# Kernel tuning notes

Hardware: AMD Instinct MI355X
Metric: run time of the kernel (lower is better)

Reference implementation:

```python
import jax, jax.numpy as jnp
import numpy as np

DIM = 1024
HEADS = 16
HEAD_DIM = DIM // HEADS


def setup_inputs() -> dict:
    key = jax.random.key(0)
    ks = jax.random.split(key, 9)
    s = 1.0 / np.sqrt(DIM)
    return {
        "x": jax.random.normal(ks[0], (2, 2048, 1, DIM), dtype=jnp.float32),
        "Wq": jax.random.normal(ks[1], (DIM, DIM), dtype=jnp.float32) * s,
        "bq": jnp.zeros((DIM,), dtype=jnp.float32),
        "Wk": jax.random.normal(ks[2], (DIM, DIM), dtype=jnp.float32) * s,
        "bk": jnp.zeros((DIM,), dtype=jnp.float32),
        "Wv": jax.random.normal(ks[3], (DIM, DIM), dtype=jnp.float32) * s,
        "bv": jnp.zeros((DIM,), dtype=jnp.float32),
        "Wo": jax.random.normal(ks[4], (DIM, DIM), dtype=jnp.float32) * s,
        "bo": jnp.zeros((DIM,), dtype=jnp.float32),
    }


def reference(x, Wq, bq, Wk, bk, Wv, bv, Wo, bo):
    b, t, _, d = x.shape
    h, hd = HEADS, HEAD_DIM
    # torch Linear: y = x @ W.T + b
    q = (x @ Wq.T + bq).reshape(b, t, h, hd)
    k = (x @ Wk.T + bk).reshape(b, t, h, hd)
    v = (x @ Wv.T + bv).reshape(b, t, h, hd)
    # Source applies self.scaling (hd**-0.5) in torch AND divides by
    # sqrt(k_features) inside the jax chunk routine -> net scale 1/hd.
    q = q * (1.0 / hd)
    # key_chunk_size >= T -> one chunk; online softmax == exact stable softmax
    scores = jnp.einsum('bqhd,bkhd->bhqk', q, k)  # [B,H,T,T]
    w = jax.nn.softmax(scores, axis=-1)
    o = jnp.einsum('bhqk,bkhd->bqhd', w, v).reshape(b, t, d)
    return o @ Wo.T + bo
```

## Files before the change

### kernel.cpp

```cpp
#include <hip/hip_runtime.h>
#include <math.h>

typedef _Float16 f16;
typedef _Float16 f16x2 __attribute__((ext_vector_type(2)));
typedef _Float16 f16x4 __attribute__((ext_vector_type(4)));
typedef _Float16 f16x8 __attribute__((ext_vector_type(8)));
typedef float    f32x4 __attribute__((ext_vector_type(4)));

constexpr int DIM   = 1024;
constexpr int HEADS = 16;
constexpr int HD    = 64;
constexpr int BATCH = 2;
constexpr int SEQ   = 2048;
constexpr int MTOT  = BATCH * SEQ;
constexpr int NT2   = SEQ / 128;

#define QSCALE (1.4426950408889634f / 64.0f)

#define MFMA16(a, b, c) __builtin_amdgcn_mfma_f32_16x16x32_f16((a), (b), (c), 0, 0, 0)
#define SPLIT2(x, hh, ll) { const float _t = (x); hh = (f16)_t; ll = (f16)(_t - (float)(hh)); }

__device__ __forceinline__ void glds16(const void* g, void* l) {
    __builtin_amdgcn_global_load_lds(
        (const __attribute__((address_space(1))) void*)g,
        (__attribute__((address_space(3))) void*)l, 16, 0, 0);
}

__device__ __forceinline__ float exp2_hw(float x) {
    float r;
    asm("v_exp_f32 %0, %1" : "=v"(r) : "v"(x));
    return r;
}

__device__ __forceinline__ f16x2 pk_f16(float a, float b) {
    return __builtin_bit_cast(f16x2, __builtin_amdgcn_cvt_pkrtz(a, b));
}

__global__ __launch_bounds__(256) void presplit_kernel(
    const float* __restrict__ x,  const float* __restrict__ Wq,
    const float* __restrict__ Wk, const float* __restrict__ Wv,
    const float* __restrict__ Wo,
    f16* __restrict__ Xh,  f16* __restrict__ WqH, f16* __restrict__ WkH,
    f16* __restrict__ WvH, f16* __restrict__ WoH, f16* __restrict__ WoL)
{
    const int bid = blockIdx.x;
    const float* src; f16* dh; f16* dl = nullptr; int row;
    if (bid < 4096)      { src = x;  dh = Xh;  row = bid; }
    else if (bid < 5120) { src = Wq; dh = WqH; row = bid - 4096; }
    else if (bid < 6144) { src = Wk; dh = WkH; row = bid - 5120; }
    else if (bid < 7168) { src = Wv; dh = WvH; row = bid - 6144; }
    else                 { src = Wo; dh = WoH; dl = WoL; row = bid - 7168; }

    const int k = threadIdx.x * 4;
    const float4 v = *reinterpret_cast<const float4*>(&src[(size_t)row * DIM + k]);
    const int s = (row >> 1) & 3;
    const size_t o = (size_t)row * DIM + (k & ~31) + ((k & 31) ^ (s << 3));
    if (dl) {
        f16x4 h4, l4;
        SPLIT2(v.x, h4[0], l4[0]); SPLIT2(v.y, h4[1], l4[1]);
        SPLIT2(v.z, h4[2], l4[2]); SPLIT2(v.w, h4[3], l4[3]);
        *reinterpret_cast<f16x4*>(&dh[o]) = h4;
        *reinterpret_cast<f16x4*>(&dl[o]) = l4;
    } else {
        f16x4 h4;
        h4[0] = (f16)v.x; h4[1] = (f16)v.y; h4[2] = (f16)v.z; h4[3] = (f16)v.w;
        *reinterpret_cast<f16x4*>(&dh[o]) = h4;
    }
}

template <int MODE, int TERMS>
__device__ __forceinline__ void gemm_plane_body(
    const f16* __restrict__ AhG, const f16* __restrict__ BhG,
    const f16* __restrict__ BlG, const float* __restrict__ bias,
    float* __restrict__ C, f16* __restrict__ F, float scale,
    f16* __restrict__ smem)
{
    f16* Ah = smem;
    f16* Bh = smem + 4096;
    f16* Bl = smem + 8192;

    const int tid = threadIdx.x;
    const int l   = tid & 63;
    const int w   = tid >> 6;
    const int wm  = (w >> 1) * 64;
    const int wn  = (w & 1) * 64;
    const int m0  = blockIdx.y * 128;
    const int n0  = blockIdx.x * 128;
    const int fr  = l & 15;
    const int fk  = (l >> 4) * 8;
    const int rg  = (l >> 4) * 4;
    const int fko = fk ^ (((fr >> 1) & 3) << 3);

    f32x4 acc[4][4] = {};

    for (int k0 = 0; k0 < DIM; k0 += 32) {
        __syncthreads();
        constexpr int NCH = (TERMS == 1) ? 4 : 6;
        #pragma unroll
        for (int j = 0; j < NCH; ++j) {
            const int c = w * NCH + j;
            const int p = c >> 3;
            const f16* P = (p == 0) ? AhG : (p == 1) ? BhG : BlG;
            const int r0 = (p == 0) ? m0 : n0;
            const int row = r0 + (c & 7) * 16 + (l >> 2);
            glds16(P + (size_t)row * DIM + k0 + (l & 3) * 8, smem + c * 512);
        }
        asm volatile("s_waitcnt vmcnt(0)" ::: "memory");
        __syncthreads();

        f16x8 ah[4], bh[4], bl[4];
        #pragma unroll
        for (int m = 0; m < 4; ++m)
            ah[m] = *reinterpret_cast<const f16x8*>(&Ah[(wm + m * 16 + fr) * 32 + fko]);
        #pragma unroll
        for (int n = 0; n < 4; ++n) {
            const int r = (wn + n * 16 + fr) * 32 + fko;
            bh[n] = *reinterpret_cast<const f16x8*>(&Bh[r]);
            if (TERMS == 2) bl[n] = *reinterpret_cast<const f16x8*>(&Bl[r]);
        }
        #pragma unroll
        for (int n = 0; n < 4; ++n) {
            #pragma unroll
            for (int m = 0; m < 4; ++m) {
                if (MODE == 1) {
                    acc[m][n] = MFMA16(bh[n], ah[m], acc[m][n]);
                } else {
                    acc[m][n] = MFMA16(ah[m], bh[n], acc[m][n]);
                    if (TERMS == 2)
                        acc[m][n] = MFMA16(ah[m], bl[n], acc[m][n]);
                }
            }
        }
    }

    if (MODE == 0 || MODE == 3) {
        #pragma unroll
        for (int n = 0; n < 4; ++n) {
            const int col  = n0 + wn + n * 16 + fr;
            const float bb = bias[col];
            #pragma unroll
            for (int m = 0; m < 4; ++m) {
                #pragma unroll
                for (int r = 0; r < 4; ++r) {
                    const int row = m0 + wm + m * 16 + rg + r;
                    const float v = (acc[m][n][r] + bb) * scale;
                    if (MODE == 0) C[(size_t)row * DIM + col] = v;
                    else           F[(size_t)row * DIM + col] = (f16)v;
                }
            }
        }
    } else if (MODE == 1) {
        constexpr int RS = 72;
        const int batch = m0 >> 11;
        const int kvg0  = m0 & 2047;
        for (int s = 0; s < 2; ++s) {
            __syncthreads();
            if ((w & 1) == s) {
                #pragma unroll
                for (int n = 0; n < 4; ++n) {
                    #pragma unroll
                    for (int m = 0; m < 4; ++m) {
                        const int kvrow = wm + m * 16 + fr;
                        const int dd    = n * 16 + rg;
                        f16x4 h4;
                        #pragma unroll
                        for (int r = 0; r < 4; ++r)
                            h4[r] = (f16)(acc[m][n][r] + bias[n0 + wn + dd + r]);
                        const int o = kvrow * RS + (dd ^ ((kvrow & 7) << 3));
                        *reinterpret_cast<f16x4*>(&smem[o]) = h4;
                    }
                }
            }
            __syncthreads();
            const size_t bh_ = (size_t)batch * HEADS + (n0 >> 6) + s;
            const int row = tid >> 1, c0 = (tid & 1) * 32;
            #pragma unroll
            for (int j = 0; j < 4; ++j) {
                const int so = row * RS + c0 + j * 8;
                const size_t go = bh_ * 131072 + (size_t)(kvg0 + row) * 64 + c0 + j * 8;
                *reinterpret_cast<f16x8*>(&F[go]) =
                    *reinterpret_cast<const f16x8*>(&smem[so]);
            }
        }
    } else {
        constexpr int RS = 136;
        const int batch = m0 >> 11;
        const int kvg0  = m0 & 2047;
        for (int s = 0; s < 2; ++s) {
            __syncthreads();
            if ((w & 1) == s) {
                #pragma unroll
                for (int n = 0; n < 4; ++n) {
                    const int d    = n * 16 + fr;
                    const float bb = bias[n0 + wn + d];
                    #pragma unroll
                    for (int m = 0; m < 4; ++m) {
                        const int kvl = wm + m * 16 + rg;
                        f16x4 h4;
                        h4[0] = (f16)(acc[m][n][0] + bb);
                        h4[1] = (f16)(acc[m][n][1] + bb);
                        h4[2] = (f16)(acc[m][n][2] + bb);
                        h4[3] = (f16)(acc[m][n][3] + bb);
                        const int o = d * RS + (kvl ^ ((d & 7) << 3));
                        *reinterpret_cast<f16x4*>(&smem[o]) = h4;
                    }
                }
            }
            __syncthreads();
            const size_t bh_ = (size_t)batch * HEADS + (n0 >> 6) + s;
            const int row = tid >> 2, c0 = (tid & 3) * 32;
            #pragma unroll
            for (int j = 0; j < 4; ++j) {
                const int so = row * RS + c0 + j * 8;
                const size_t go = bh_ * 131072 + (size_t)row * 2048 + kvg0 + c0 + j * 8;
                *reinterpret_cast<f16x8*>(&F[go]) =
                    *reinterpret_cast<const f16x8*>(&smem[so]);
            }
        }
    }
}

__global__ __launch_bounds__(256) void qkv_kernel(
    const f16* __restrict__ XhG,
    const f16* __restrict__ WqH, const float* __restrict__ bq,
    const f16* __restrict__ WkH, const float* __restrict__ bk,
    const f16* __restrict__ WvH, const float* __restrict__ bv,
    f16* __restrict__ QhG, f16* __restrict__ KhG, f16* __restrict__ VhG)
{
    __shared__ __align__(16) f16 smem[9216];
    if (blockIdx.z == 0)
        gemm_plane_body<3, 1>(XhG, WqH, nullptr, bq, nullptr, QhG, QSCALE, smem);
    else if (blockIdx.z == 1)
        gemm_plane_body<1, 1>(XhG, WkH, nullptr, bk, nullptr, KhG, 1.0f, smem);
    else
        gemm_plane_body<2, 1>(XhG, WvH, nullptr, bv, nullptr, VhG, 1.0f, smem);
}

__global__ __launch_bounds__(256) void oproj_kernel(
    const f16* __restrict__ OhG,
    const f16* __restrict__ WoH, const f16* __restrict__ WoL,
    const float* __restrict__ bo, float* __restrict__ out)
{
    __shared__ __align__(16) f16 smem[12288];
    gemm_plane_body<0, 2>(OhG, WoH, WoL, bo, out, nullptr, 1.0f, smem);
}

__global__ __launch_bounds__(256, 2) void attn_kernel(
    const f16* __restrict__ QhG, const f16* __restrict__ KhG,
    const f16* __restrict__ VhG, f16* __restrict__ OhG)
{
    __shared__ __align__(16) f16 lds[2][2][8192];
    __shared__ __align__(16) f16 PL[4][2][1024];

    const int tid = threadIdx.x;
    const int l   = tid & 63;
    const int w   = tid >> 6;
    const int fr  = l & 15;
    const int g   = l >> 4;
    const int fk  = g * 8;
    const int rg  = g * 4;
    const int swz = (fr & 7) << 3;

    const int lin  = blockIdx.x + 16 * (blockIdx.y + 16 * blockIdx.z);
    const int sid  = (lin & 7) * 64 + (lin >> 3);
    const int qblk = sid & 15;
    const int head = (sid >> 4) & 15;
    const int batch = sid >> 8;

    const int q0 = qblk * 128;
    const size_t rowbase = (size_t)batch * SEQ;
    const int hcol = head * HD;
    const size_t bhbase = ((size_t)batch * HEADS + head) * (size_t)(SEQ * HD);

    size_t kA[4], vA[4];
    #pragma unroll
    for (int c = 0; c < 4; ++c) {
        const int h0 = (w * 4 + c) * 512 + l * 8;
        kA[c] = bhbase + (size_t)h0;
        vA[c] = bhbase + (size_t)(h0 >> 7) * 2048 + (h0 & 127);
    }

#define STAGE(B, T) do {                                                    \
        const size_t _ko = (size_t)(T) * 8192;                              \
        const size_t _vo = (size_t)(T) * 128;                               \
        _Pragma("unroll")                                                   \
        for (int c = 0; c < 4; ++c) {                                       \
            const int lo_ = (w * 4 + c) * 512;                              \
            glds16(KhG + kA[c] + _ko, &lds[B][0][lo_]);                     \
            glds16(VhG + vA[c] + _vo, &lds[B][1][lo_]);                     \
        }                                                                   \
    } while (0)

    STAGE(0, 0);

    f16x8 qh[2][2];
    #pragma unroll
    for (int qb = 0; qb < 2; ++qb) {
        const f16* qp = &QhG[(rowbase + q0 + w * 32 + qb * 16 + fr) * DIM + hcol];
        qh[qb][0] = *reinterpret_cast<const f16x8*>(&qp[fk]);
        qh[qb][1] = *reinterpret_cast<const f16x8*>(&qp[32 + fk]);
    }

    f16x8 onesv;
    #pragma unroll
    for (int i = 0; i < 8; ++i) onesv[i] = (f16)1.0f;

    f32x4 ls[2] = {};
    f32x4 oa[4][2] = {};

    int cur = 0;
    for (int t = 0; t < NT2; ++t) {
        asm volatile("s_waitcnt vmcnt(0) lgkmcnt(0)\ns_barrier" ::: "memory");
        if (t + 1 < NT2) STAGE(cur ^ 1, t + 1);

        #pragma unroll
        for (int hh = 0; hh < 2; ++hh) {
            const f16* Kh = &lds[cur][0][hh * 4096];
            const f16* Vh = &lds[cur][1][hh * 64];

            f32x4 sa[4][2] = {};
            __builtin_amdgcn_s_setprio(1);
            #pragma unroll
            for (int kvb = 0; kvb < 4; ++kvb) {
                #pragma unroll
                for (int ks = 0; ks < 2; ++ks) {
                    const int o = ((kvb * 16 + fr) * 64 + ks * 32 + fk) ^ swz;
                    const f16x8 kh = *reinterpret_cast<const f16x8*>(&Kh[o]);
                    sa[kvb][0] = MFMA16(kh, qh[0][ks], sa[kvb][0]);
                    sa[kvb][1] = MFMA16(kh, qh[1][ks], sa[kvb][1]);
                }
            }
            __builtin_amdgcn_s_setprio(0);

            f16x8 pf[2][2];
            #pragma unroll
            for (int qb = 0; qb < 2; ++qb) {
                f16* Wh = &PL[w][qb][0];
                #pragma unroll
                for (int kvb = 0; kvb < 4; ++kvb) {
                    const f16x2 p01 = pk_f16(exp2_hw(sa[kvb][qb][0]),
                                             exp2_hw(sa[kvb][qb][1]));
                    const f16x2 p23 = pk_f16(exp2_hw(sa[kvb][qb][2]),
                                             exp2_hw(sa[kvb][qb][3]));
                    f16x4 h4;
                    h4[0] = p01[0]; h4[1] = p01[1]; h4[2] = p23[0]; h4[3] = p23[1];
                    const int po = (fr * 64 + kvb * 16 + rg) ^ swz;
                    *reinterpret_cast<f16x4*>(&Wh[po]) = h4;
                }
                #pragma unroll
                for (int ks = 0; ks < 2; ++ks) {
                    const int ro = (fr * 64 + ks * 32 + fk) ^ swz;
                    pf[qb][ks] = *reinterpret_cast<const f16x8*>(&Wh[ro]);
                }
            }

            __builtin_amdgcn_s_setprio(1);
            #pragma unroll
            for (int qb = 0; qb < 2; ++qb)
                #pragma unroll
                for (int ks = 0; ks < 2; ++ks)
                    ls[qb] = MFMA16(onesv, pf[qb][ks], ls[qb]);
            #pragma unroll
            for (int db = 0; db < 4; ++db) {
                #pragma unroll
                for (int ks = 0; ks < 2; ++ks) {
                    const int vo = (db * 16 + fr) * 128 + ((ks * 32 + fk) ^ swz);
                    const f16x8 vh = *reinterpret_cast<const f16x8*>(&Vh[vo]);
                    oa[db][0] = MFMA16(vh, pf[0][ks], oa[db][0]);
                    oa[db][1] = MFMA16(vh, pf[1][ks], oa[db][1]);
                }
            }
            __builtin_amdgcn_s_setprio(0);
        }
        cur ^= 1;
    }
#undef STAGE

    #pragma unroll
    for (int qb = 0; qb < 2; ++qb) {
        const float inv = 1.0f / ls[qb][0];
        const size_t row = rowbase + q0 + w * 32 + qb * 16 + fr;
        const int s = ((int)row >> 1) & 3;
        #pragma unroll
        for (int db = 0; db < 4; ++db) {
            f16x4 h4;
            #pragma unroll
            for (int j = 0; j < 4; ++j) h4[j] = (f16)(oa[db][qb][j] * inv);
            const int kg = hcol + db * 16 + rg;
            const size_t o = row * DIM + (kg & ~31) + ((kg & 31) ^ (s << 3));
            *reinterpret_cast<f16x4*>(&OhG[o]) = h4;
        }
    }
}

extern "C" void kernel_launch(void* const* d_in, const int* in_sizes, int n_in,
                              void* d_out, int out_size, void* d_ws, size_t ws_size,
                              hipStream_t stream)
{
    const float* x  = (const float*)d_in[0];
    const float* Wq = (const float*)d_in[1];
    const float* bq = (const float*)d_in[2];
    const float* Wk = (const float*)d_in[3];
    const float* bk = (const float*)d_in[4];
    const float* Wv = (const float*)d_in[5];
    const float* bv = (const float*)d_in[6];
    const float* Wo = (const float*)d_in[7];
    const float* bo = (const float*)d_in[8];
    float* out = (float*)d_out;

    const size_t PS = (size_t)MTOT * DIM;
    f16* QhG = (f16*)d_ws;
    f16* KhG = QhG + PS;
    f16* VhG = KhG + PS;
    f16* XhG = VhG + PS;
    f16* WqH = XhG + PS;
    f16* WkH = WqH + (size_t)DIM * DIM;
    f16* WvH = WkH + (size_t)DIM * DIM;
    f16* WoH = WvH + (size_t)DIM * DIM;
    f16* WoL = WoH + (size_t)DIM * DIM;
    f16* OhG = XhG;

    presplit_kernel<<<8192, 256, 0, stream>>>(x, Wq, Wk, Wv, Wo,
                                              XhG, WqH, WkH, WvH, WoH, WoL);

    dim3 gqkv(DIM / 128, MTOT / 128, 3);
    qkv_kernel<<<gqkv, 256, 0, stream>>>(XhG, WqH, bq, WkH, bk, WvH, bv,
                                         QhG, KhG, VhG);

    dim3 gattn(SEQ / 128, HEADS, BATCH);
    attn_kernel<<<gattn, 256, 0, stream>>>(QhG, KhG, VhG, OhG);

    dim3 gout(DIM / 128, MTOT / 128);
    oproj_kernel<<<gout, 256, 0, stream>>>(OhG, WoH, WoL, bo, out);
}
```

Baseline: 125.9 us.

## Double-buffer LDS tiles in projection GEMM main loop

Restructures the shared GEMM body used by the QKV and output projections so the next K-slice is loaded asynchronously into a second LDS buffer while MFMAs run on the current one. One barrier per iteration replaces the previous two, and global-load latency can overlap with compute. In exchange it doubles LDS per block for both kernels, which may reduce occupancy.

```diff
diff --git a/kernel.cpp b/kernel.cpp
--- a/kernel.cpp
+++ b/kernel.cpp
@@ -75,9 +75,8 @@
     float* __restrict__ C, f16* __restrict__ F, float scale,
     f16* __restrict__ smem)
 {
-    f16* Ah = smem;
-    f16* Bh = smem + 4096;
-    f16* Bl = smem + 8192;
+    constexpr int NCH  = (TERMS == 1) ? 4 : 6;
+    constexpr int BUFH = NCH * 4 * 512;
 
     const int tid = threadIdx.x;
     const int l   = tid & 63;
@@ -93,20 +92,29 @@
 
     f32x4 acc[4][4] = {};
 
+#define GSTAGE(B, K0) do {                                                  \
+        _Pragma("unroll")                                                   \
+        for (int j = 0; j < NCH; ++j) {                                     \
+            const int c = w * NCH + j;                                      \
+            const int p = c >> 3;                     \
+            const f16* P = (p == 0) ? AhG : (p == 1) ? BhG : BlG;           \
+            const int r0 = (p == 0) ? m0 : n0;                              \
+            const int row = r0 + (c & 7) * 16 + (l >> 2);                   \
+            glds16(P + (size_t)row * DIM + (K0) + (l & 3) * 8,              \
+                   smem + (B) * BUFH + c * 512);                            \
+        }                                                                   \
+    } while (0)
+
+    GSTAGE(0, 0);
+    asm volatile("s_waitcnt vmcnt(0)\ns_barrier" ::: "memory");
+    int cur = 0;
+
     for (int k0 = 0; k0 < DIM; k0 += 32) {
-        __syncthreads();
-        constexpr int NCH = (TERMS == 1) ? 4 : 6;
-        #pragma unroll
-        for (int j = 0; j < NCH; ++j) {
-            const int c = w * NCH + j;
-            const int p = c >> 3;
-            const f16* P = (p == 0) ? AhG : (p == 1) ? BhG : BlG;
-            const int r0 = (p == 0) ? m0 : n0;
-            const int row = r0 + (c & 7) * 16 + (l >> 2);
-            glds16(P + (size_t)row * DIM + k0 + (l & 3) * 8, smem + c * 512);
-        }
-        asm volatile("s_waitcnt vmcnt(0)" ::: "memory");
-        __syncthreads();
+        if (k0 + 32 < DIM) GSTAGE(cur ^ 1, k0 + 32);
+
+        const f16* Ah = smem + cur * BUFH;
+        const f16* Bh = Ah + 4096;
+        const f16* Bl = Bh + 4096;
 
         f16x8 ah[4], bh[4], bl[4];
         #pragma unroll
@@ -131,7 +139,10 @@
                 }
             }
         }
-    }
+        asm volatile("s_waitcnt vmcnt(0) lgkmcnt(0)\ns_barrier" ::: "memory");
+        cur ^= 1;
+    }
+#undef GSTAGE
 
     if (MODE == 0 || MODE == 3) {
         #pragma unroll
@@ -227,7 +238,7 @@
     const f16* __restrict__ WvH, const float* __restrict__ bv,
     f16* __restrict__ QhG, f16* __restrict__ KhG, f16* __restrict__ VhG)
 {
-    __shared__ __align__(16) f16 smem[9216];
+    __shared__ __align__(16) f16 smem[18432];
     if (blockIdx.z == 0)
         gemm_plane_body<3, 1>(XhG, WqH, nullptr, bq, nullptr, QhG, QSCALE, smem);
     else if (blockIdx.z == 1)
@@ -241,7 +252,7 @@
     const f16* __restrict__ WoH, const f16* __restrict__ WoL,
     const float* __restrict__ bo, float* __restrict__ out)
 {
-    __shared__ __align__(16) f16 smem[12288];
+    __shared__ __align__(16) f16 smem[24576];
     gemm_plane_body<0, 2>(OhG, WoH, WoL, bo, out, nullptr, 1.0f, smem);
 }
 
```

Result: slower. 132.2 us (+5.0%).

## Drop split-fp16 Wo low term and deepen GEMM K-tile to 64

Applied to the files above, without the earlier changes.

The output projection no longer keeps a high/low fp16 split of Wo. It now uses only the fp16 high part, which halves the MFMA count and removes the WoL buffer and its writes in the presplit kernel. The shared GEMM body also moves from a K-step of 32 to 64, loading twice as much per iteration into larger LDS tiles to halve the number of barrier/wait rounds. The cost is lower output-projection precision and more LDS use per block, with a possible rise in bank conflicts from the wider 64-element row stride.

```diff
diff --git a/kernel.cpp b/kernel.cpp
--- a/kernel.cpp
+++ b/kernel.cpp
@@ -18,7 +18,6 @@
 #define QSCALE (1.4426950408889634f / 64.0f)
 
 #define MFMA16(a, b, c) __builtin_amdgcn_mfma_f32_16x16x32_f16((a), (b), (c), 0, 0, 0)
-#define SPLIT2(x, hh, ll) { const float _t = (x); hh = (f16)_t; ll = (f16)(_t - (float)(hh)); }
 
 __device__ __forceinline__ void glds16(const void* g, void* l) {
     __builtin_amdgcn_global_load_lds(
@@ -41,43 +40,33 @@
     const float* __restrict__ Wk, const float* __restrict__ Wv,
     const float* __restrict__ Wo,
     f16* __restrict__ Xh,  f16* __restrict__ WqH, f16* __restrict__ WkH,
-    f16* __restrict__ WvH, f16* __restrict__ WoH, f16* __restrict__ WoL)
+    f16* __restrict__ WvH, f16* __restrict__ WoH)
 {
     const int bid = blockIdx.x;
-    const float* src; f16* dh; f16* dl = nullptr; int row;
+    const float* src; f16* dh; int row;
     if (bid < 4096)      { src = x;  dh = Xh;  row = bid; }
     else if (bid < 5120) { src = Wq; dh = WqH; row = bid - 4096; }
     else if (bid < 6144) { src = Wk; dh = WkH; row = bid - 5120; }
     else if (bid < 7168) { src = Wv; dh = WvH; row = bid - 6144; }
-    else                 { src = Wo; dh = WoH; dl = WoL; row = bid - 7168; }
+    else                 { src = Wo; dh = WoH; row = bid - 7168; }
 
     const int k = threadIdx.x * 4;
     const float4 v = *reinterpret_cast<const float4*>(&src[(size_t)row * DIM + k]);
     const int s = (row >> 1) & 3;
     const size_t o = (size_t)row * DIM + (k & ~31) + ((k & 31) ^ (s << 3));
-    if (dl) {
-        f16x4 h4, l4;
-        SPLIT2(v.x, h4[0], l4[0]); SPLIT2(v.y, h4[1], l4[1]);
-        SPLIT2(v.z, h4[2], l4[2]); SPLIT2(v.w, h4[3], l4[3]);
-        *reinterpret_cast<f16x4*>(&dh[o]) = h4;
-        *reinterpret_cast<f16x4*>(&dl[o]) = l4;
-    } else {
-        f16x4 h4;
-        h4[0] = (f16)v.x; h4[1] = (f16)v.y; h4[2] = (f16)v.z; h4[3] = (f16)v.w;
-        *reinterpret_cast<f16x4*>(&dh[o]) = h4;
-    }
-}
-
-template <int MODE, int TERMS>
+    f16x4 h4;
+    h4[0] = (f16)v.x; h4[1] = (f16)v.y; h4[2] = (f16)v.z; h4[3] = (f16)v.w;
+    *reinterpret_cast<f16x4*>(&dh[o]) = h4;
+}
+
+template <int MODE>
 __device__ __forceinline__ void gemm_plane_body(
     const f16* __restrict__ AhG, const f16* __restrict__ BhG,
-    const f16* __restrict__ BlG, const float* __restrict__ bias,
-    float* __restrict__ C, f16* __restrict__ F, float scale,
-    f16* __restrict__ smem)
+    const float* __restrict__ bias, float* __restrict__ C,
+    f16* __restrict__ F, float scale, f16* __restrict__ smem)
 {
     f16* Ah = smem;
-    f16* Bh = smem + 4096;
-    f16* Bl = smem + 8192;
+    f16* Bh = smem + 8192;
 
     const int tid = threadIdx.x;
     const int l   = tid & 63;
@@ -93,44 +82,44 @@
 
     f32x4 acc[4][4] = {};
 
-    for (int k0 = 0; k0 < DIM; k0 += 32) {
+    for (int k0 = 0; k0 < DIM; k0 += 64) {
         __syncthreads();
-        constexpr int NCH = (TERMS == 1) ? 4 : 6;
-        #pragma unroll
-        for (int j = 0; j < NCH; ++j) {
-            const int c = w * NCH + j;
-            const int p = c >> 3;
-            const f16* P = (p == 0) ? AhG : (p == 1) ? BhG : BlG;
+        #pragma unroll
+        for (int j = 0; j < 8; ++j) {
+            const int c  = w * 8 + j;
+            const int p  = c >> 4;
+            const int cc = c & 15;
+            const f16* P = (p == 0) ? AhG : BhG;
             const int r0 = (p == 0) ? m0 : n0;
-            const int row = r0 + (c & 7) * 16 + (l >> 2);
-            glds16(P + (size_t)row * DIM + k0 + (l & 3) * 8, smem + c * 512);
+            const int row = r0 + cc * 8 + (l >> 3);
+            glds16(P + (size_t)row * DIM + k0 + (l & 7) * 8, smem + c * 512);
         }
         asm volatile("s_waitcnt vmcnt(0)" ::: "memory");
         __syncthreads();
 
-        f16x8 ah[4], bh[4], bl[4];
-        #pragma unroll
-        for (int m = 0; m < 4; ++m)
-            ah[m] = *reinterpret_cast<const f16x8*>(&Ah[(wm + m * 16 + fr) * 32 + fko]);
-        #pragma unroll
-        for (int n = 0; n < 4; ++n) {
-            const int r = (wn + n * 16 + fr) * 32 + fko;
-            bh[n] = *reinterpret_cast<const f16x8*>(&Bh[r]);
-            if (TERMS == 2) bl[n] = *reinterpret_cast<const f16x8*>(&Bl[r]);
-        }
-        #pragma unroll
-        for (int n = 0; n < 4; ++n) {
-            #pragma unroll
-            for (int m = 0; m < 4; ++m) {
-                if (MODE == 1) {
-                    acc[m][n] = MFMA16(bh[n], ah[m], acc[m][n]);
-                } else {
-                    acc[m][n] = MFMA16(ah[m], bh[n], acc[m][n]);
-                    if (TERMS == 2)
-                        acc[m][n] = MFMA16(ah[m], bl[n], acc[m][n]);
-                }
-            }
-        }
+        f16x8 ah[2][4], bh[2][4];
+        #pragma unroll
+        for (int ks = 0; ks < 2; ++ks) {
+            #pragma unroll
+            for (int m = 0; m < 4; ++m)
+                ah[ks][m] = *reinterpret_cast<const f16x8*>(
+                    &Ah[(wm + m * 16 + fr) * 64 + ks * 32 + fko]);
+            #pragma unroll
+            for (int n = 0; n < 4; ++n)
+                bh[ks][n] = *reinterpret_cast<const f16x8*>(
+                    &Bh[(wn + n * 16 + fr) * 64 + ks * 32 + fko]);
+        }
+        #pragma unroll
+        for (int ks = 0; ks < 2; ++ks)
+            #pragma unroll
+            for (int n = 0; n < 4; ++n)
+                #pragma unroll
+                for (int m = 0; m < 4; ++m) {
+                    if (MODE == 1)
+                        acc[m][n] = MFMA16(bh[ks][n], ah[ks][m], acc[m][n]);
+                    else
+                        acc[m][n] = MFMA16(ah[ks][m], bh[ks][n], acc[m][n]);
+                }
     }
 
     if (MODE == 0 || MODE == 3) {
@@ -227,22 +216,21 @@
     const f16* __restrict__ WvH, const float* __restrict__ bv,
     f16* __restrict__ QhG, f16* __restrict__ KhG, f16* __restrict__ VhG)
 {
-    __shared__ __align__(16) f16 smem[9216];
+    __shared__ __align__(16) f16 smem[18432];
     if (blockIdx.z == 0)
-        gemm_plane_body<3, 1>(XhG, WqH, nullptr, bq, nullptr, QhG, QSCALE, smem);
+        gemm_plane_body<3>(XhG, WqH, bq, nullptr, QhG, QSCALE, smem);
     else if (blockIdx.z == 1)
-        gemm_plane_body<1, 1>(XhG, WkH, nullptr, bk, nullptr, KhG, 1.0f, smem);
+        gemm_plane_body<1>(XhG, WkH, bk, nullptr, KhG, 1.0f, smem);
     else
-        gemm_plane_body<2, 1>(XhG, WvH, nullptr, bv, nullptr, VhG, 1.0f, smem);
+        gemm_plane_body<2>(XhG, WvH, bv, nullptr, VhG, 1.0f, smem);
 }
 
 __global__ __launch_bounds__(256) void oproj_kernel(
-    const f16* __restrict__ OhG,
-    const f16* __restrict__ WoH, const f16* __restrict__ WoL,
+    const f16* __restrict__ OhG, const f16* __restrict__ WoH,
     const float* __restrict__ bo, float* __restrict__ out)
 {
-    __shared__ __align__(16) f16 smem[12288];
-    gemm_plane_body<0, 2>(OhG, WoH, WoL, bo, out, nullptr, 1.0f, smem);
+    __shared__ __align__(16) f16 smem[16384];
+    gemm_plane_body<0>(OhG, WoH, bo, out, nullptr, 1.0f, smem);
 }
 
 __global__ __launch_bounds__(256, 2) void attn_kernel(
@@ -417,11 +405,10 @@
     f16* WkH = WqH + (size_t)DIM * DIM;
     f16* WvH = WkH + (size_t)DIM * DIM;
     f16* WoH = WvH + (size_t)DIM * DIM;
-    f16* WoL = WoH + (size_t)DIM * DIM;
     f16* OhG = XhG;
 
     presplit_kernel<<<8192, 256, 0, stream>>>(x, Wq, Wk, Wv, Wo,
-                                              XhG, WqH, WkH, WvH, WoH, WoL);
+                                              XhG, WqH, WkH, WvH, WoH);
 
     dim3 gqkv(DIM / 128, MTOT / 128, 3);
     qkv_kernel<<<gqkv, 256, 0, stream>>>(XhG, WqH, bq, WkH, bk, WvH, bv,
@@ -431,5 +418,5 @@
     attn_kernel<<<gattn, 256, 0, stream>>>(QhG, KhG, VhG, OhG);
 
     dim3 gout(DIM / 128, MTOT / 128);
-    oproj_kernel<<<gout, 256, 0, stream>>>(OhG, WoH, WoL, bo, out);
-}
+    oproj_kernel<<<gout, 256, 0, stream>>>(OhG, WoH, bo, out);
+}
```

After: 124.7 us. About the same (-1.0%).
